# Performance work log

Hardware: AMD Instinct MI355X
Metric: run time of the kernel (lower is better)

Reference implementation:

```python
import jax, jax.numpy as jnp
import numpy as np

N = 512       # nodes
V = 8         # n_vectors_hidden
F = 128       # n_invariant_feat_hidden
H = 8         # num_heads
BESSEL = 8
R_MAX = 10.0
FH = F // H
VH = V // H

def _edges(n):
    s, r = np.meshgrid(np.arange(n), np.arange(n), indexing='ij')
    m = s != r
    return jnp.asarray(s[m], jnp.int32), jnp.asarray(r[m], jnp.int32)

def _sph(v):
    # real spherical harmonics ell=1,2,3, e3nn 'component' normalization, unit input v[...,3] -> [...,15]
    x, y, z = v[..., 0], v[..., 1], v[..., 2]
    s3, s15, s5 = np.sqrt(3.0), np.sqrt(15.0), np.sqrt(5.0)
    sh1 = jnp.stack([x, y, z], -1) * s3
    sh2 = jnp.stack([s15 * x * y, s15 * y * z, 0.5 * s5 * (3 * z**2 - 1), s15 * x * z, 0.5 * s15 * (x**2 - y**2)], -1)
    c33, c32, c31, c30 = np.sqrt(35.0 / 8.0), np.sqrt(105.0), np.sqrt(21.0 / 8.0), 0.5 * np.sqrt(7.0)
    sh3 = jnp.stack([c33 * y * (3 * x**2 - y**2), c32 * x * y * z, c31 * y * (5 * z**2 - 1), c30 * z * (5 * z**2 - 3), c31 * x * (5 * z**2 - 1), 0.5 * c32 * z * (x**2 - y**2), c33 * x * (x**2 - 3 * y**2)], -1)
    return jnp.concatenate([sh1, sh2, sh3], -1)

def _bessel(x, n, x_max):
    # e3nn.bessel basis: sqrt(2/x_max) * sin(k*pi*x/x_max) / x, k=1..n
    x = x[..., None]
    k = jnp.arange(1, n + 1, dtype=x.dtype)
    x_safe = jnp.where(x == 0, 1.0, x)
    return np.sqrt(2.0 / x_max) * jnp.sin(k * jnp.pi * x / x_max) / x_safe

def _sus(x):
    return jnp.where(x > 0, jnp.exp(-1.0 / jnp.where(x > 0, x, 1.0)), 0.0)

def _soft_envelope(x, x_max, a=2.0, v0=1.2):
    return v0 * _sus(a * (1.0 - x / x_max)) / _sus(jnp.asarray(a, x.dtype))

def _forward(positions, features, We0, be0, We1, be1, Wq, Wk, Wek, Wv, Wev, Wg, Wo0, bo0, Wo1, bo1, Wo2, bo2):
    n = positions.shape[0]
    senders, receivers = _edges(n)
    vec = positions[senders] - positions[receivers]               # [E,V,3] gather
    lengths = jnp.sqrt(jnp.sum(vec * vec, -1) + 1e-20)            # safe_norm [E,V]
    unit = vec / lengths[..., None]
    sph = _sph(unit)                                              # [E,V,15]
    radial = _bessel(lengths, BESSEL, R_MAX) * _soft_envelope(lengths, R_MAX)[..., None]  # [E,V,B]
    e_scal = radial.reshape(radial.shape[0], -1)                  # [E, V*B]
    h = jax.nn.silu(e_scal @ We0 + be0)
    h = jax.nn.silu(h @ We1 + be1)                                # edge MLP, output_activation=silu
    E = h.shape[0]
    q = (features @ Wq).reshape(n, H, FH)
    k = (features[senders] @ Wk + h @ Wek).reshape(E, H, FH)
    logits = jnp.einsum('ehf,ehf->eh', q[receivers], k) / np.sqrt(FH)
    seg_max = jax.ops.segment_max(logits, receivers, num_segments=n)
    ex = jnp.exp(logits - seg_max[receivers])                     # edge_weight_cutoff = 1
    denom = jax.ops.segment_sum(ex, receivers, num_segments=n)
    alpha = ex / denom[receivers]                                 # [E,H] per-receiver softmax
    v_s = (features[senders] @ Wv + h @ Wev).reshape(E, H, FH)
    gate = h @ Wg                                                 # [E,V] invariant gates
    v_vec = (gate[..., None] * sph[..., :3]).reshape(E, H, VH, 3) # equivariant values from ell=1 sph
    agg_s = jax.ops.segment_sum(alpha[..., None] * v_s, receivers, num_segments=n).reshape(n, F)
    agg_v = jax.ops.segment_sum(alpha[:, :, None, None] * v_vec, receivers, num_segments=n).reshape(n, V, 3)
    o = jax.nn.silu(agg_s @ Wo0 + bo0)
    o = jax.nn.silu(o @ Wo1 + bo1)
    o = o @ Wo2 + bo2                                             # hk MLP: last layer linear
    return (positions + agg_v, features + o)

def setup_inputs() -> dict:
    key = jax.random.key(0)
    ks = jax.random.split(key, 16)
    def w(k, i, o):
        return jax.random.normal(k, (i, o), jnp.float32) / np.sqrt(i)
    M = 128
    D = V * BESSEL
    return {
        'positions': jax.random.normal(ks[0], (N, V, 3), jnp.float32),
        'features': jax.random.normal(ks[1], (N, F), jnp.float32),
        'We0': w(ks[2], D, M), 'be0': jnp.zeros((M,), jnp.float32),
        'We1': w(ks[3], M, M), 'be1': jnp.zeros((M,), jnp.float32),
        'Wq': w(ks[4], F, F), 'Wk': w(ks[5], F, F), 'Wek': w(ks[6], M, F),
        'Wv': w(ks[7], F, F), 'Wev': w(ks[8], M, F), 'Wg': w(ks[9], M, V),
        'Wo0': w(ks[10], F, M), 'bo0': jnp.zeros((M,), jnp.float32),
        'Wo1': w(ks[11], M, M), 'bo1': jnp.zeros((M,), jnp.float32),
        'Wo2': w(ks[12], M, F), 'bo2': jnp.zeros((F,), jnp.float32),
    }

def reference(positions, features, We0, be0, We1, be1, Wq, Wk, Wek, Wv, Wev, Wg, Wo0, bo0, Wo1, bo1, Wo2, bo2):
    return _forward(positions, features, We0, be0, We1, be1, Wq, Wk, Wek, Wv, Wev, Wg, Wo0, bo0, Wo1, bo1, Wo2, bo2)
```

## Files before the change

### kernel.cpp

```cpp
#include <hip/hip_runtime.h>
#include <hip/hip_bf16.h>

#define WS_KNB  0
#define WS_VNT  32768
#define WS_AW2  65536
#define WS_W0T  1114112
#define WS_W1T  1118208
#define WS_PS   1126400
#define PS_STRIDE 1072

typedef short bf16x8 __attribute__((ext_vector_type(8)));
typedef short short4v __attribute__((ext_vector_type(4)));
typedef float f32x4 __attribute__((ext_vector_type(4)));
typedef unsigned short ushort_t;

static __device__ __forceinline__ ushort_t f2b(float x) {
  __hip_bfloat16 h = __float2bfloat16(x);
  return reinterpret_cast<ushort_t&>(h);
}
static __device__ __forceinline__ float b2f(ushort_t u) {
  unsigned v = ((unsigned)u) << 16;
  return reinterpret_cast<float&>(v);
}
static __device__ __forceinline__ float fsilu(float x) {
  return x * __builtin_amdgcn_rcpf(1.f + __expf(-x));
}

static __device__ __forceinline__ bf16x8 radial_frag(
    float dx, float dy, float dz, float& ux, float& uy, float& uz)
{
  const float l2 = fmaf(dx,dx, fmaf(dy,dy, fmaf(dz,dz, 1e-20f)));
  const float inv = rsqrtf(l2);
  const float len = l2 * inv;
  ux = dx*inv; uy = dy*inv; uz = dz*inv;
  const float yy = 2.f - len*0.2f;
  const float env = (yy > 0.f) ? 1.9784655648f * __expf(-__builtin_amdgcn_rcpf(yy)) : 0.f;
  const float coef = 0.4472135955f * env * inv;
  const float arg = len * 0.31415926535f;
  const float s1v = __sinf(arg), c1v = __cosf(arg);
  const float twc = 2.f*c1v;
  float sp = 0.f, sc = s1v;
  bf16x8 ev;
#pragma unroll
  for (int bb = 0; bb < 8; ++bb) {
    ev[bb] = (short)f2b(coef*sc);
    const float nx = fmaf(twc, sc, -sp);
    sp = sc; sc = nx;
  }
  return ev;
}

__global__ __launch_bounds__(128) void k_prep(
    const float* __restrict__ feat, const float* __restrict__ Wq,
    const float* __restrict__ Wk, const float* __restrict__ Wv,
    const float* __restrict__ Wek, const float* __restrict__ Wg,
    const float* __restrict__ We0, const float* __restrict__ We1,
    float* __restrict__ ws)
{
  const int blk = blockIdx.x, j = threadIdx.x;
  if (blk >= 512) {
    const int i = (blk - 512)*128 + j;
    ushort_t* W0T = (ushort_t*)(ws + WS_W0T);
    ushort_t* W1T = (ushort_t*)(ws + WS_W1T);
    if (i < 8192) {
      const int n = i >> 6, k = i & 63;
      W0T[n*64 + k] = f2b(We0[k*128 + n]);
    } else {
      const int t = i - 8192, n = t >> 7, k = t & 127;
      W1T[n*128 + k] = f2b(We1[k*128 + n]);
    }
    return;
  }
  const int r = blk;
  __shared__ float fr[128];
  __shared__ float qL[128];
  fr[j] = feat[r*128 + j];
  __syncthreads();
  float aq = 0.f, ak = 0.f, av = 0.f;
#pragma unroll 4
  for (int i = 0; i < 128; ++i) {
    const float f = fr[i];
    aq = fmaf(f, Wq[i*128 + j], aq);
    ak = fmaf(f, Wk[i*128 + j], ak);
    av = fmaf(f, Wv[i*128 + j], av);
  }
  ushort_t* knB = (ushort_t*)(ws + WS_KNB);
  ushort_t* vnT = (ushort_t*)(ws + WS_VNT);
  knB[r*128 + j] = f2b(ak);
  vnT[j*512 + r] = f2b(av);
  qL[j] = aq;
  __syncthreads();
  ushort_t* AW = (ushort_t*)(ws + WS_AW2) + r*4096;
  const float* wr = Wek + j*128;
  const int jh = j >> 4;
#pragma unroll
  for (int h = 0; h < 8; ++h) {
    float acc = 0.f;
#pragma unroll
    for (int f = 0; f < 16; ++f)
      acc = fmaf(wr[16*h + f], qL[16*h + f], acc);
    AW[h*256 + j] = f2b(acc * 0.25f);
    AW[h*256 + 128 + j] = (h == jh) ? f2b(0.25f * aq) : (ushort_t)0;
  }
#pragma unroll
  for (int v = 0; v < 8; ++v) {
    AW[(8 + v)*256 + j] = f2b(Wg[j*8 + v]);
    AW[(8 + v)*256 + 128 + j] = 0;
  }
}

#define MFMA(a,b,c) __builtin_amdgcn_mfma_f32_16x16x32_bf16((a),(b),(c),0,0,0)

__global__ __launch_bounds__(512, 4) void k_edge11(
    const float* __restrict__ pos,
    const float* __restrict__ be0, const float* __restrict__ be1,
    float* __restrict__ ws)
{
  __shared__ __align__(16) char Lds[40960];
  ushort_t* H1   = (ushort_t*)(Lds);
  ushort_t* Pb   = (ushort_t*)(Lds);
  float*    rscL = (float*)(Lds + 2048);
  ushort_t* H2t  = (ushort_t*)(Lds + 16384);
  ushort_t* Es   = (ushort_t*)(Lds + 32768);
  float*    lgT0 = (float*)(Lds + 32768);
  float*    lgT1 = (float*)(Lds + 36864);

  const int tid = threadIdx.x;
  const int nw = tid >> 6, l = tid & 63;
  const int c = l & 15, g = l >> 4;
  const int b = blockIdx.x;
  const int r = b >> 1, half = b & 1;
  const int base = half * 256;

  const ushort_t* knB = (const ushort_t*)(ws + WS_KNB);
  const ushort_t* vnT = (const ushort_t*)(ws + WS_VNT);
  const ushort_t* AW2 = (const ushort_t*)(ws + WS_AW2) + r*4096;
  const ushort_t* W0T = (const ushort_t*)(ws + WS_W0T);
  const ushort_t* W1T = (const ushort_t*)(ws + WS_W1T);

  const int ncol = nw*16 + c;
  const float be0v = be0[ncol], be1v = be1[ncol];
  const int m_lg = nw & 3, kh = nw >> 2;

  const float prx = pos[r*24 + nw*3 + 0];
  const float pry = pos[r*24 + nw*3 + 1];
  const float prz = pos[r*24 + nw*3 + 2];

  f32x4 bh = {0,0,0,0}, sna = {0,0,0,0};
  float avx = 0.f, avy = 0.f, avz = 0.f;
  float mrun = -1e30f, drun = 0.f;
  float ux, uy, uz;

  {
    const int sg = base + l;
    const bf16x8 ev = radial_frag(pos[sg*24 + nw*3 + 0] - prx,
                                  pos[sg*24 + nw*3 + 1] - pry,
                                  pos[sg*24 + nw*3 + 2] - prz, ux, uy, uz);
    *(bf16x8*)(Es + l*64 + ((nw ^ (l&7))<<3)) = ev;
  }
  __syncthreads();

  for (int tile = 0; tile < 4; ++tile) {
    const int gbase = base + tile*64;

    float npx = 0.f, npy = 0.f, npz = 0.f;
    if (tile < 3) {
      const int sg = gbase + 64 + l;
      npx = pos[sg*24 + nw*3 + 0];
      npy = pos[sg*24 + nw*3 + 1];
      npz = pos[sg*24 + nw*3 + 2];
    }

    {
      const bf16x8 w0f0 = *(const bf16x8*)(W0T + ncol*64 + g*8);
      const bf16x8 w0f1 = *(const bf16x8*)(W0T + ncol*64 + 32 + g*8);
#pragma unroll
      for (int m = 0; m < 4; ++m) {
        const int ra = m*16 + c;
        const bf16x8 e0 = *(const bf16x8*)(Es + ra*64 + (((g  ) ^ (ra&7))<<3));
        const bf16x8 e1 = *(const bf16x8*)(Es + ra*64 + (((4+g) ^ (ra&7))<<3));
        f32x4 acc = {0,0,0,0};
        acc = MFMA(e0, w0f0, acc);
        acc = MFMA(e1, w0f1, acc);
#pragma unroll
        for (int i = 0; i < 4; ++i) {
          const int row = m*16 + g*4 + i;
          H1[row*128 + (((ncol>>3) ^ (row&15))<<3) + (c&7)] =
              f2b(fsilu(acc[i] + be0v));
        }
      }
    }
    __syncthreads();

#pragma unroll
    for (int m = 0; m < 4; ++m) {
      const int ra = m*16 + c;
      f32x4 acc = {0,0,0,0};
#pragma unroll
      for (int kb = 0; kb < 4; ++kb) {
        const bf16x8 af = *(const bf16x8*)(H1 + ra*128 + (((kb*4+g) ^ (ra&15))<<3));
        const bf16x8 wf = *(const bf16x8*)(W1T + ncol*128 + kb*32 + g*8);
        acc = MFMA(af, wf, acc);
      }
      short4v pk;
#pragma unroll
      for (int i = 0; i < 4; ++i)
        pk[i] = (short)f2b(fsilu(acc[i] + be1v));
      *(short4v*)(H2t + ncol*64 + (((m*2 + (g>>1)) ^ (ncol&7))<<3) + (g&1)*4) = pk;
    }
    __syncthreads();

    {
      f32x4 lg = {0,0,0,0};
      if (kh == 0) {
        const int rb = m_lg*2 + (c>>3);
        const int rl = c & 7;
#pragma unroll
        for (int kb = 0; kb < 4; ++kb) {
          bf16x8 bb;
#pragma unroll
          for (int j = 0; j < 8; ++j)
            bb[j] = (short)H2t[(kb*32 + g*8 + j)*64 + ((rb ^ j)<<3) + rl];
          const bf16x8 aw = *(const bf16x8*)(AW2 + c*256 + kb*32 + g*8);
          lg = MFMA(aw, bb, lg);
        }
      } else {
        const int srow = gbase + m_lg*16 + c;
#pragma unroll
        for (int kb = 0; kb < 4; ++kb) {
          const bf16x8 bb = *(const bf16x8*)(knB + srow*128 + kb*32 + g*8);
          const bf16x8 aw = *(const bf16x8*)(AW2 + c*256 + 128 + kb*32 + g*8);
          lg = MFMA(aw, bb, lg);
        }
      }
      float* lgW = kh ? lgT1 : lgT0;
#pragma unroll
      for (int i = 0; i < 4; ++i) {
        const int ch = g*4 + i;
        lgW[ch*64 + ((m_lg*16 + c) ^ (g<<4))] = lg[i];
      }
    }
    __syncthreads();

    {
      const int h = nw;
      const int kv = (h>>2)<<4;
      const int kg = ((8+h)>>2)<<4;
      float lgv = lgT0[h*64 + (l ^ kv)] + lgT1[h*64 + (l ^ kv)];
      const float gate = lgT0[(8+h)*64 + (l ^ kg)] + lgT1[(8+h)*64 + (l ^ kg)];
      if (gbase + l == r) lgv = -1e30f;
      float t = lgv;
      t = fmaxf(t, __shfl_xor(t, 1));
      t = fmaxf(t, __shfl_xor(t, 2));
      t = fmaxf(t, __shfl_xor(t, 4));
      t = fmaxf(t, __shfl_xor(t, 8));
      t = fmaxf(t, __shfl_xor(t, 16));
      t = fmaxf(t, __shfl_xor(t, 32));
      const float mnew = fmaxf(mrun, t);
      const float rsc = __expf(mrun - mnew);
      mrun = mnew;
      const float val = __expf(lgv - mnew);
      float wsm = val;
      wsm += __shfl_xor(wsm, 1);
      wsm += __shfl_xor(wsm, 2);
      wsm += __shfl_xor(wsm, 4);
      wsm += __shfl_xor(wsm, 8);
      wsm += __shfl_xor(wsm, 16);
      wsm += __shfl_xor(wsm, 32);
      drun = drun*rsc + wsm;
      const float ga = val * gate;
      Pb[h*64 + (((l>>3) ^ h)<<3) + (l&7)] = f2b(val);
      Pb[(8+h)*64 + (((l>>3) ^ h)<<3) + (l&7)] = f2b(ga);
      if (l == 0) rscL[h] = rsc;
      avx = avx*rsc + ga*ux;
      avy = avy*rsc + ga*uy;
      avz = avz*rsc + ga*uz;
    }
    __syncthreads();

    {
      float rs[4];
#pragma unroll
      for (int i = 0; i < 4; ++i) rs[i] = rscL[(4*g + i) & 7];
#pragma unroll
      for (int i = 0; i < 4; ++i) { bh[i] *= rs[i]; sna[i] *= rs[i]; }
      const bf16x8 pa0 = *(const bf16x8*)(Pb + c*64 + (((g  ) ^ (c&7))<<3));
      const bf16x8 pa1 = *(const bf16x8*)(Pb + c*64 + (((4+g) ^ (c&7))<<3));
      bh = MFMA(pa0, *(const bf16x8*)(H2t + ncol*64 + (((g  ) ^ (ncol&7))<<3)), bh);
      bh = MFMA(pa1, *(const bf16x8*)(H2t + ncol*64 + (((4+g) ^ (ncol&7))<<3)), bh);
      const bf16x8 vnf0 = *(const bf16x8*)(vnT + ncol*512 + gbase + g*8);
      const bf16x8 vnf1 = *(const bf16x8*)(vnT + ncol*512 + gbase + 32 + g*8);
      sna = MFMA(pa0, vnf0, sna);
      sna = MFMA(pa1, vnf1, sna);
    }
    if (tile < 3) {
      const bf16x8 ev = radial_frag(npx - prx, npy - pry, npz - prz, ux, uy, uz);
      *(bf16x8*)(Es + l*64 + ((nw ^ (l&7))<<3)) = ev;
      __syncthreads();
    }
  }

  float* PSf = ws + WS_PS + b*PS_STRIDE;
  ushort_t* PSs = (ushort_t*)PSf;
  if (g < 2) {
#pragma unroll
    for (int i = 0; i < 4; ++i) {
      PSs[(4*g + i)*128 + ncol] = f2b(bh[i]);
      PSs[1024 + (4*g + i)*128 + ncol] = f2b(sna[i]);
    }
  }
  avx += __shfl_xor(avx, 1); avy += __shfl_xor(avy, 1); avz += __shfl_xor(avz, 1);
  avx += __shfl_xor(avx, 2); avy += __shfl_xor(avy, 2); avz += __shfl_xor(avz, 2);
  avx += __shfl_xor(avx, 4); avy += __shfl_xor(avy, 4); avz += __shfl_xor(avz, 4);
  avx += __shfl_xor(avx, 8); avy += __shfl_xor(avy, 8); avz += __shfl_xor(avz, 8);
  avx += __shfl_xor(avx,16); avy += __shfl_xor(avy,16); avz += __shfl_xor(avz,16);
  avx += __shfl_xor(avx,32); avy += __shfl_xor(avy,32); avz += __shfl_xor(avz,32);
  if (l == 0) {
    PSf[1024 + nw*3 + 0] = avx;
    PSf[1024 + nw*3 + 1] = avy;
    PSf[1024 + nw*3 + 2] = avz;
    PSf[1048 + nw] = mrun;
    PSf[1056 + nw] = drun;
  }
}

__global__ __launch_bounds__(128) void k_merge(
    const float* __restrict__ pos, const float* __restrict__ feat,
    const float* __restrict__ Wev,
    const float* __restrict__ Wo0, const float* __restrict__ bo0,
    const float* __restrict__ Wo1, const float* __restrict__ bo1,
    const float* __restrict__ Wo2, const float* __restrict__ bo2,
    const float* __restrict__ ws, float* __restrict__ out)
{
  const int r = blockIdx.x, j = threadIdx.x;
  __shared__ float S1s[8], S2s[8], Dh[8];
  __shared__ float BhC[1024];
  __shared__ float asB[128], o1[128], o2[128];
  const float* P1f = ws + WS_PS + (2*r)*PS_STRIDE;
  const float* P2f = P1f + PS_STRIDE;
  const ushort_t* P1s = (const ushort_t*)P1f;
  const ushort_t* P2s = (const ushort_t*)P2f;
  if (j < 8) {
    const float m1 = P1f[1048 + j], m2 = P2f[1048 + j];
    const float M = fmaxf(m1, m2);
    const float s1 = __expf(m1 - M), s2 = __expf(m2 - M);
    S1s[j] = s1; S2s[j] = s2;
    Dh[j] = s1*P1f[1056 + j] + s2*P2f[1056 + j];
  }
  __syncthreads();
#pragma unroll
  for (int h = 0; h < 8; ++h)
    BhC[h*128 + j] = S1s[h]*b2f(P1s[h*128 + j]) + S2s[h]*b2f(P2s[h*128 + j]);
  const int hh = j >> 4;
  const float snj = S1s[hh]*b2f(P1s[1024 + hh*128 + j])
                  + S2s[hh]*b2f(P2s[1024 + hh*128 + j]);
  if (j < 24) {
    const int v = j / 3;
    const float avc = S1s[v]*P1f[1024 + j] + S2s[v]*P2f[1024 + j];
    out[r*24 + j] = pos[r*24 + j]
        + 1.7320508076f * avc * __builtin_amdgcn_rcpf(Dh[v]);
  }
  __syncthreads();
  {
    float ev = 0.f;
#pragma unroll 4
    for (int m = 0; m < 128; ++m)
      ev = fmaf(BhC[hh*128 + m], Wev[m*128 + j], ev);
    asB[j] = (snj + ev) * __builtin_amdgcn_rcpf(Dh[hh]);
  }
  __syncthreads();
  {
    float acc = bo0[j];
#pragma unroll 4
    for (int i = 0; i < 128; ++i) acc = fmaf(asB[i], Wo0[i*128 + j], acc);
    o1[j] = fsilu(acc);
  }
  __syncthreads();
  {
    float acc = bo1[j];
#pragma unroll 4
    for (int i = 0; i < 128; ++i) acc = fmaf(o1[i], Wo1[i*128 + j], acc);
    o2[j] = fsilu(acc);
  }
  __syncthreads();
  {
    float acc = bo2[j];
#pragma unroll 4
    for (int i = 0; i < 128; ++i) acc = fmaf(o2[i], Wo2[i*128 + j], acc);
    out[12288 + r*128 + j] = feat[r*128 + j] + acc;
  }
}

extern "C" void kernel_launch(void* const* d_in, const int* in_sizes, int n_in,
                              void* d_out, int out_size, void* d_ws, size_t ws_size,
                              hipStream_t stream)
{
  const float* pos  = (const float*)d_in[0];
  const float* feat = (const float*)d_in[1];
  const float* We0  = (const float*)d_in[2];
  const float* be0  = (const float*)d_in[3];
  const float* We1  = (const float*)d_in[4];
  const float* be1  = (const float*)d_in[5];
  const float* Wq   = (const float*)d_in[6];
  const float* Wk   = (const float*)d_in[7];
  const float* Wek  = (const float*)d_in[8];
  const float* Wv   = (const float*)d_in[9];
  const float* Wev  = (const float*)d_in[10];
  const float* Wg   = (const float*)d_in[11];
  const float* Wo0  = (const float*)d_in[12];
  const float* bo0  = (const float*)d_in[13];
  const float* Wo1  = (const float*)d_in[14];
  const float* bo1  = (const float*)d_in[15];
  const float* Wo2  = (const float*)d_in[16];
  const float* bo2  = (const float*)d_in[17];
  float* ws  = (float*)d_ws;
  float* out = (float*)d_out;

  hipLaunchKernelGGL(k_prep, dim3(704), dim3(128), 0, stream,
                     feat, Wq, Wk, Wv, Wek, Wg, We0, We1, ws);
  hipLaunchKernelGGL(k_edge11, dim3(1024), dim3(512), 0, stream,
                     pos, be0, be1, ws);
  hipLaunchKernelGGL(k_merge, dim3(512), dim3(128), 0, stream,
                     pos, feat, Wev, Wo0, bo0, Wo1, bo1, Wo2, bo2, ws, out);
}
```

Before: 103.1 us.

## Prefetch key/value fragments early, add MFMA priority hints, reswizzle H2t LDS layout

Moves the global loads of key fragments and value fragments ahead of the preceding GEMM and barrier so their latency overlaps compute. Wraps MFMA sections in s_setprio to favour matrix issue across waves. Changes the XOR swizzle of the transposed H2 tile to also depend on the column block, which is meant to reduce LDS bank conflicts on the strided gather reads. The cost is higher register pressure from the prefetched fragments under a 4-waves launch bound.

```diff
diff --git a/kernel.cpp b/kernel.cpp
--- a/kernel.cpp
+++ b/kernel.cpp
@@ -111,7 +111,7 @@
 
 #define MFMA(a,b,c) __builtin_amdgcn_mfma_f32_16x16x32_bf16((a),(b),(c),0,0,0)
 
-__global__ __launch_bounds__(512, 4) void k_edge11(
+__global__ __launch_bounds__(512, 4) void k_edge12(
     const float* __restrict__ pos,
     const float* __restrict__ be0, const float* __restrict__ be1,
     float* __restrict__ ws)
@@ -141,6 +141,7 @@
   const int ncol = nw*16 + c;
   const float be0v = be0[ncol], be1v = be1[ncol];
   const int m_lg = nw & 3, kh = nw >> 2;
+  const int ncswz = ((ncol & 7) ^ ((ncol >> 3) & 7)) & 7;
 
   const float prx = pos[r*24 + nw*3 + 0];
   const float pry = pos[r*24 + nw*3 + 1];
@@ -174,6 +175,7 @@
     {
       const bf16x8 w0f0 = *(const bf16x8*)(W0T + ncol*64 + g*8);
       const bf16x8 w0f1 = *(const bf16x8*)(W0T + ncol*64 + 32 + g*8);
+      __builtin_amdgcn_s_setprio(1);
 #pragma unroll
       for (int m = 0; m < 4; ++m) {
         const int ra = m*16 + c;
@@ -182,16 +184,27 @@
         f32x4 acc = {0,0,0,0};
         acc = MFMA(e0, w0f0, acc);
         acc = MFMA(e1, w0f1, acc);
+        __builtin_amdgcn_s_setprio(0);
 #pragma unroll
         for (int i = 0; i < 4; ++i) {
           const int row = m*16 + g*4 + i;
           H1[row*128 + (((ncol>>3) ^ (row&15))<<3) + (c&7)] =
               f2b(fsilu(acc[i] + be0v));
         }
+        __builtin_amdgcn_s_setprio(1);
       }
+      __builtin_amdgcn_s_setprio(0);
     }
     __syncthreads();
 
+    bf16x8 knf[4];
+    if (kh == 1) {
+      const int srow = gbase + m_lg*16 + c;
+#pragma unroll
+      for (int kb = 0; kb < 4; ++kb)
+        knf[kb] = *(const bf16x8*)(knB + srow*128 + kb*32 + g*8);
+    }
+    __builtin_amdgcn_s_setprio(1);
 #pragma unroll
     for (int m = 0; m < 4; ++m) {
       const int ra = m*16 + c;
@@ -202,36 +215,46 @@
         const bf16x8 wf = *(const bf16x8*)(W1T + ncol*128 + kb*32 + g*8);
         acc = MFMA(af, wf, acc);
       }
+      __builtin_amdgcn_s_setprio(0);
       short4v pk;
 #pragma unroll
       for (int i = 0; i < 4; ++i)
         pk[i] = (short)f2b(fsilu(acc[i] + be1v));
-      *(short4v*)(H2t + ncol*64 + (((m*2 + (g>>1)) ^ (ncol&7))<<3) + (g&1)*4) = pk;
-    }
+      *(short4v*)(H2t + ncol*64 +
+          ((((m*2 + (g>>1)) ^ ncswz) & 7)<<3) + (g&1)*4) = pk;
+      __builtin_amdgcn_s_setprio(1);
+    }
+    __builtin_amdgcn_s_setprio(0);
     __syncthreads();
 
+    const bf16x8 vnf0 = *(const bf16x8*)(vnT + ncol*512 + gbase + g*8);
+    const bf16x8 vnf1 = *(const bf16x8*)(vnT + ncol*512 + gbase + 32 + g*8);
     {
       f32x4 lg = {0,0,0,0};
       if (kh == 0) {
         const int rb = m_lg*2 + (c>>3);
         const int rl = c & 7;
+        __builtin_amdgcn_s_setprio(1);
 #pragma unroll
         for (int kb = 0; kb < 4; ++kb) {
+          const int cc = (kb*4 + g) & 7;
           bf16x8 bb;
 #pragma unroll
           for (int j = 0; j < 8; ++j)
-            bb[j] = (short)H2t[(kb*32 + g*8 + j)*64 + ((rb ^ j)<<3) + rl];
+            bb[j] = (short)H2t[(kb*32 + g*8 + j)*64 +
+                               (((rb ^ j ^ cc) & 7)<<3) + rl];
           const bf16x8 aw = *(const bf16x8*)(AW2 + c*256 + kb*32 + g*8);
           lg = MFMA(aw, bb, lg);
         }
+        __builtin_amdgcn_s_setprio(0);
       } else {
-        const int srow = gbase + m_lg*16 + c;
+        __builtin_amdgcn_s_setprio(1);
 #pragma unroll
         for (int kb = 0; kb < 4; ++kb) {
-          const bf16x8 bb = *(const bf16x8*)(knB + srow*128 + kb*32 + g*8);
           const bf16x8 aw = *(const bf16x8*)(AW2 + c*256 + 128 + kb*32 + g*8);
-          lg = MFMA(aw, bb, lg);
+          lg = MFMA(aw, knf[kb], lg);
         }
+        __builtin_amdgcn_s_setprio(0);
       }
       float* lgW = kh ? lgT1 : lgT0;
 #pragma unroll
@@ -286,12 +309,14 @@
       for (int i = 0; i < 4; ++i) { bh[i] *= rs[i]; sna[i] *= rs[i]; }
       const bf16x8 pa0 = *(const bf16x8*)(Pb + c*64 + (((g  ) ^ (c&7))<<3));
       const bf16x8 pa1 = *(const bf16x8*)(Pb + c*64 + (((4+g) ^ (c&7))<<3));
-      bh = MFMA(pa0, *(const bf16x8*)(H2t + ncol*64 + (((g  ) ^ (ncol&7))<<3)), bh);
-      bh = MFMA(pa1, *(const bf16x8*)(H2t + ncol*64 + (((4+g) ^ (ncol&7))<<3)), bh);
-      const bf16x8 vnf0 = *(const bf16x8*)(vnT + ncol*512 + gbase + g*8);
-      const bf16x8 vnf1 = *(const bf16x8*)(vnT + ncol*512 + gbase + 32 + g*8);
+      __builtin_amdgcn_s_setprio(1);
+      bh = MFMA(pa0, *(const bf16x8*)(H2t + ncol*64 +
+               ((((g  ) ^ ncswz) & 7)<<3)), bh);
+      bh = MFMA(pa1, *(const bf16x8*)(H2t + ncol*64 +
+               ((((4+g) ^ ncswz) & 7)<<3)), bh);
       sna = MFMA(pa0, vnf0, sna);
       sna = MFMA(pa1, vnf1, sna);
+      __builtin_amdgcn_s_setprio(0);
     }
     if (tile < 3) {
       const bf16x8 ev = radial_frag(npx - prx, npy - pry, npz - prz, ux, uy, uz);
@@ -418,7 +443,7 @@
 
   hipLaunchKernelGGL(k_prep, dim3(704), dim3(128), 0, stream,
                      feat, Wq, Wk, Wv, Wek, Wg, We0, We1, ws);
-  hipLaunchKernelGGL(k_edge11, dim3(1024), dim3(512), 0, stream,
+  hipLaunchKernelGGL(k_edge12, dim3(1024), dim3(512), 0, stream,
                      pos, be0, be1, ws);
   hipLaunchKernelGGL(k_merge, dim3(512), dim3(128), 0, stream,
                      pos, feat, Wev, Wo0, bo0, Wo1, bo1, Wo2, bo2, ws, out);
```

Measured after the change: 143.7 us. 1.39x slower.
